# Performance work log

Measured on AMD Instinct MI355X. Metric: run time of the kernel, lower is better.

## Reference

```python
import jax, jax.numpy as jnp
import numpy as np

BATCH = 4096
DIM = 512
TEMP = 0.5

def setup_inputs() -> dict:
    key = jax.random.key(0)
    k1, k2 = jax.random.split(key)
    emb_i = jax.random.normal(k1, (BATCH, DIM), dtype=jnp.float32)
    emb_j = jax.random.normal(k2, (BATCH, DIM), dtype=jnp.float32)
    return {"emb_i": emb_i, "emb_j": emb_j}

def reference(emb_i, emb_j):
    n = emb_i.shape[0]
    # L2-normalize once (torch F.normalize uses eps=1e-12 clamp on norm)
    z_i = emb_i / jnp.maximum(jnp.linalg.norm(emb_i, axis=1, keepdims=True), 1e-12)
    z_j = emb_j / jnp.maximum(jnp.linalg.norm(emb_j, axis=1, keepdims=True), 1e-12)
    z = jnp.concatenate([z_i, z_j], axis=0)            # [2N, D]
    sim = jnp.einsum('nd,md->nm', z, z)                # cosine sim, single GEMM
    # positives: diag(sim, +N) and diag(sim, -N) == rowwise dot(z_i, z_j)
    pos_ij = jnp.sum(z_i * z_j, axis=1)                # [N]
    positives = jnp.concatenate([pos_ij, pos_ij], 0)   # [2N]
    exp_sim = jnp.exp(sim / TEMP)
    mask = 1.0 - jnp.eye(2 * n, dtype=sim.dtype)
    denom = jnp.sum(mask * exp_sim, axis=1)            # [2N]
    loss_partial = -(positives / TEMP - jnp.log(denom))
    return jnp.sum(loss_partial) / (2 * n)
```

## Files before the change

### kernel.cpp

```cpp
#include <hip/hip_runtime.h>
#include <hip/hip_bf16.h>

#define N_ROWS 4096
#define DIM 512
#define TWO_N 8192
#define NTILE 64
#define NTRI  (NTILE * (NTILE + 1) / 2)

typedef __bf16 bf16x8 __attribute__((ext_vector_type(8)));
typedef float  f32x4  __attribute__((ext_vector_type(4)));

__device__ inline unsigned short f2bf(float f) {
    unsigned int u = __float_as_uint(f);
    u += 0x7fffu + ((u >> 16) & 1u);
    return (unsigned short)(u >> 16);
}

__device__ inline void g2l16(const void* g, void* l) {
    __builtin_amdgcn_global_load_lds(
        (const __attribute__((address_space(1))) void*)g,
        (__attribute__((address_space(3))) void*)l,
        16, 0, 0);
}

__global__ void normalize_kernel(const float* __restrict__ ei,
                                 const float* __restrict__ ej,
                                 unsigned short* __restrict__ zb,
                                 float* __restrict__ pos,
                                 float* __restrict__ denom,
                                 float* __restrict__ out) {
    int r = blockIdx.x;
    int t = threadIdx.x;
    const float2 vi = ((const float2*)(ei + (size_t)r * DIM))[t];
    const float2 vj = ((const float2*)(ej + (size_t)r * DIM))[t];
    float si  = vi.x * vi.x + vi.y * vi.y;
    float sj  = vj.x * vj.x + vj.y * vj.y;
    float sij = vi.x * vj.x + vi.y * vj.y;

    for (int o = 32; o; o >>= 1) {
        si  += __shfl_down(si, o);
        sj  += __shfl_down(sj, o);
        sij += __shfl_down(sij, o);
    }
    __shared__ float red[3][4];
    int wave = t >> 6, lane = t & 63;
    if (lane == 0) { red[0][wave] = si; red[1][wave] = sj; red[2][wave] = sij; }
    __syncthreads();
    si  = red[0][0] + red[0][1] + red[0][2] + red[0][3];
    sj  = red[1][0] + red[1][1] + red[1][2] + red[1][3];
    sij = red[2][0] + red[2][1] + red[2][2] + red[2][3];

    float rni = 1.0f / fmaxf(sqrtf(si), 1e-12f);
    float rnj = 1.0f / fmaxf(sqrtf(sj), 1e-12f);
    if (t == 0) {
        pos[r] = sij * rni * rnj;
        denom[r] = 0.0f;
        denom[r + N_ROWS] = 0.0f;
        if (r == 0) out[0] = 0.0f;
    }
    ushort2 zi2 = make_ushort2(f2bf(vi.x * rni), f2bf(vi.y * rni));
    ushort2 zj2 = make_ushort2(f2bf(vj.x * rnj), f2bf(vj.y * rnj));
    ((ushort2*)(zb + (size_t)r * DIM))[t] = zi2;
    ((ushort2*)(zb + (size_t)(r + N_ROWS) * DIM))[t] = zj2;
}

__global__ __launch_bounds__(256, 4) void gemm_exp_kernel(
        const unsigned short* __restrict__ zb,
        float* __restrict__ denom) {
    const int w = blockIdx.x;
    const int t = (w & 7) * (NTRI / 8) + (w >> 3);
    int by = (int)(0.5f * (2.0f * NTILE + 1.0f -
              sqrtf((2.0f * NTILE + 1.0f) * (2.0f * NTILE + 1.0f) - 8.0f * t)));
    while ((by + 1) * NTILE - ((by + 1) * by) / 2 <= t) ++by;
    while (by * NTILE - (by * (by - 1)) / 2 > t) --by;
    const int bx = by + (t - (by * NTILE - (by * (by - 1)) / 2));

    const int rb = by * 128, cb = bx * 128;
    const bool diag = (rb == cb);

    const int tid  = threadIdx.x;
    const int wave = tid >> 6;
    const int lane = tid & 63;
    const int quad = lane >> 4;
    const int m    = lane & 15;
    const int wm   = (wave >> 1) * 64;
    const int wn   = (wave & 1) * 64;

    __shared__ __align__(16) unsigned short As[128 * 64];
    __shared__ __align__(16) unsigned short Bs[128 * 64];

    f32x4 acc[4][4];
    #pragma unroll
    for (int i = 0; i < 4; ++i)
        #pragma unroll
        for (int j = 0; j < 4; ++j)
            #pragma unroll
            for (int r = 0; r < 4; ++r) acc[i][j][r] = 0.0f;

    const int srow8 = lane >> 3;
    const int sk    = (((lane & 7) ^ srow8) * 8);

    for (int it = 0; it < DIM / 64; ++it) {
        if (it) __syncthreads();
        const int k0 = it * 64;
        #pragma unroll
        for (int cc = 0; cc < 4; ++cc) {
            int c   = 4 * wave + cc;
            int row = c * 8 + srow8;
            g2l16(zb + (size_t)(rb + row) * DIM + k0 + sk, As + c * 512);
            g2l16(zb + (size_t)(cb + row) * DIM + k0 + sk, Bs + c * 512);
        }
        __syncthreads();

        #pragma unroll
        for (int h = 0; h < 2; ++h) {
            bf16x8 af[4], bfr[4];
            const int sl = ((((h << 2) | quad) ^ (m & 7)) * 8);
            #pragma unroll
            for (int i = 0; i < 4; ++i)
                af[i] = *(const bf16x8*)(As + (wm + i * 16 + m) * 64 + sl);
            #pragma unroll
            for (int j = 0; j < 4; ++j)
                bfr[j] = *(const bf16x8*)(Bs + (wn + j * 16 + m) * 64 + sl);

            #pragma unroll
            for (int i = 0; i < 4; ++i)
                #pragma unroll
                for (int j = 0; j < 4; ++j)
                    acc[i][j] = __builtin_amdgcn_mfma_f32_16x16x32_bf16(
                        af[i], bfr[j], acc[i][j], 0, 0, 0);
        }
    }

    __syncthreads();

    float* rs = (float*)As;
    float* cs = rs + 128;
    if (tid < 128) { rs[tid] = 0.0f; cs[tid] = 0.0f; }
    __syncthreads();

    float colsum[4] = {0.0f, 0.0f, 0.0f, 0.0f};
    #pragma unroll
    for (int i = 0; i < 4; ++i) {
        #pragma unroll
        for (int r = 0; r < 4; ++r) {
            int lrow = wm + i * 16 + quad * 4 + r;
            int grow = rb + lrow;
            float s = 0.0f;
            #pragma unroll
            for (int j = 0; j < 4; ++j) {
                int gcol = cb + wn + j * 16 + m;
                float v  = __expf(2.0f * acc[i][j][r]);
                v = (grow == gcol) ? 0.0f : v;
                s += v;
                colsum[j] += v;
            }
            s += __shfl_xor(s, 1);
            s += __shfl_xor(s, 2);
            s += __shfl_xor(s, 4);
            s += __shfl_xor(s, 8);
            if (m == 0) atomicAdd(&rs[lrow], s);
        }
    }
    if (!diag) {
        #pragma unroll
        for (int j = 0; j < 4; ++j) {
            float s = colsum[j];
            s += __shfl_xor(s, 16);
            s += __shfl_xor(s, 32);
            if (quad == 0) atomicAdd(&cs[wn + j * 16 + m], s);
        }
    }
    __syncthreads();
    if (tid < 128) {
        atomicAdd(&denom[rb + tid], rs[tid]);
        if (!diag) atomicAdd(&denom[cb + tid], cs[tid]);
    }
}

__global__ void loss_kernel(const float* __restrict__ pos,
                            const float* __restrict__ denom,
                            float* __restrict__ out) {
    int r = blockIdx.x * 256 + threadIdx.x;
    float s = __logf(denom[r]) - 2.0f * pos[r & (N_ROWS - 1)];
    for (int o = 32; o; o >>= 1) s += __shfl_down(s, o);
    __shared__ float red[4];
    int t = threadIdx.x;
    if ((t & 63) == 0) red[t >> 6] = s;
    __syncthreads();
    if (t == 0)
        atomicAdd(out, (red[0] + red[1] + red[2] + red[3]) / (float)TWO_N);
}

extern "C" void kernel_launch(void* const* d_in, const int* in_sizes, int n_in,
                              void* d_out, int out_size, void* d_ws, size_t ws_size,
                              hipStream_t stream) {
    const float* ei = (const float*)d_in[0];
    const float* ej = (const float*)d_in[1];

    unsigned short* zb  = (unsigned short*)d_ws;
    float* pos   = (float*)((char*)d_ws + (size_t)TWO_N * DIM * sizeof(unsigned short));
    float* denom = pos + N_ROWS;
    float* out   = (float*)d_out;

    normalize_kernel<<<N_ROWS, 256, 0, stream>>>(ei, ej, zb, pos, denom, out);
    gemm_exp_kernel<<<NTRI, 256, 0, stream>>>(zb, denom);
    loss_kernel<<<TWO_N / 256, 256, 0, stream>>>(pos, denom, out);
}
```

Measured before the change: 119.2 us.

## Quantize normalized embeddings to FP8 and use FP8 MFMA for similarity GEMM

Normalized embeddings are now stored as FP8 (e4m3 via cvt_pk_fp8) instead of BF16. The GEMM uses 16x16x32 fp8 MFMA with a 128-byte K tile, so there are half as many K iterations, and global and LDS traffic is halved. The trade is lower precision in the cosine similarities. Because the values are exponentiated with 1/T = 2, the loss may drift beyond tolerance.

```diff
diff --git a/kernel.cpp b/kernel.cpp
--- a/kernel.cpp
+++ b/kernel.cpp
@@ -7,14 +7,7 @@
 #define NTILE 64
 #define NTRI  (NTILE * (NTILE + 1) / 2)
 
-typedef __bf16 bf16x8 __attribute__((ext_vector_type(8)));
-typedef float  f32x4  __attribute__((ext_vector_type(4)));
-
-__device__ inline unsigned short f2bf(float f) {
-    unsigned int u = __float_as_uint(f);
-    u += 0x7fffu + ((u >> 16) & 1u);
-    return (unsigned short)(u >> 16);
-}
+typedef float f32x4 __attribute__((ext_vector_type(4)));
 
 __device__ inline void g2l16(const void* g, void* l) {
     __builtin_amdgcn_global_load_lds(
@@ -25,7 +18,7 @@
 
 __global__ void normalize_kernel(const float* __restrict__ ei,
                                  const float* __restrict__ ej,
-                                 unsigned short* __restrict__ zb,
+                                 unsigned char* __restrict__ zq,
                                  float* __restrict__ pos,
                                  float* __restrict__ denom,
                                  float* __restrict__ out) {
@@ -58,14 +51,14 @@
         denom[r + N_ROWS] = 0.0f;
         if (r == 0) out[0] = 0.0f;
     }
-    ushort2 zi2 = make_ushort2(f2bf(vi.x * rni), f2bf(vi.y * rni));
-    ushort2 zj2 = make_ushort2(f2bf(vj.x * rnj), f2bf(vj.y * rnj));
-    ((ushort2*)(zb + (size_t)r * DIM))[t] = zi2;
-    ((ushort2*)(zb + (size_t)(r + N_ROWS) * DIM))[t] = zj2;
+    int pi8 = __builtin_amdgcn_cvt_pk_fp8_f32(vi.x * rni, vi.y * rni, 0, false);
+    int pj8 = __builtin_amdgcn_cvt_pk_fp8_f32(vj.x * rnj, vj.y * rnj, 0, false);
+    ((unsigned short*)(zq + (size_t)r * DIM))[t] = (unsigned short)pi8;
+    ((unsigned short*)(zq + (size_t)(r + N_ROWS) * DIM))[t] = (unsigned short)pj8;
 }
 
 __global__ __launch_bounds__(256, 4) void gemm_exp_kernel(
-        const unsigned short* __restrict__ zb,
+        const unsigned char* __restrict__ zq,
         float* __restrict__ denom) {
     const int w = blockIdx.x;
     const int t = (w & 7) * (NTRI / 8) + (w >> 3);
@@ -86,8 +79,8 @@
     const int wm   = (wave >> 1) * 64;
     const int wn   = (wave & 1) * 64;
 
-    __shared__ __align__(16) unsigned short As[128 * 64];
-    __shared__ __align__(16) unsigned short Bs[128 * 64];
+    __shared__ __align__(16) unsigned char As[128 * 128];
+    __shared__ __align__(16) unsigned char Bs[128 * 128];
 
     f32x4 acc[4][4];
     #pragma unroll
@@ -98,36 +91,37 @@
             for (int r = 0; r < 4; ++r) acc[i][j][r] = 0.0f;
 
     const int srow8 = lane >> 3;
-    const int sk    = (((lane & 7) ^ srow8) * 8);
-
-    for (int it = 0; it < DIM / 64; ++it) {
+    const int sk    = (((lane & 7) ^ srow8) * 16);
+
+    for (int it = 0; it < 4; ++it) {
         if (it) __syncthreads();
-        const int k0 = it * 64;
+        const int k0 = it * 128;
         #pragma unroll
         for (int cc = 0; cc < 4; ++cc) {
             int c   = 4 * wave + cc;
             int row = c * 8 + srow8;
-            g2l16(zb + (size_t)(rb + row) * DIM + k0 + sk, As + c * 512);
-            g2l16(zb + (size_t)(cb + row) * DIM + k0 + sk, Bs + c * 512);
+            g2l16(zq + (size_t)(rb + row) * DIM + k0 + sk, As + c * 1024);
+            g2l16(zq + (size_t)(cb + row) * DIM + k0 + sk, Bs + c * 1024);
         }
         __syncthreads();
 
         #pragma unroll
-        for (int h = 0; h < 2; ++h) {
-            bf16x8 af[4], bfr[4];
-            const int sl = ((((h << 2) | quad) ^ (m & 7)) * 8);
+        for (int kk = 0; kk < 4; ++kk) {
+            const int s8 = kk * 4 + quad;
+            const int sl = (((s8 >> 1) ^ (m & 7)) * 16) + (s8 & 1) * 8;
+            long long af[4], bfr[4];
             #pragma unroll
             for (int i = 0; i < 4; ++i)
-                af[i] = *(const bf16x8*)(As + (wm + i * 16 + m) * 64 + sl);
+                af[i] = *(const long long*)(As + (wm + i * 16 + m) * 128 + sl);
             #pragma unroll
             for (int j = 0; j < 4; ++j)
-                bfr[j] = *(const bf16x8*)(Bs + (wn + j * 16 + m) * 64 + sl);
+                bfr[j] = *(const long long*)(Bs + (wn + j * 16 + m) * 128 + sl);
 
             #pragma unroll
             for (int i = 0; i < 4; ++i)
                 #pragma unroll
                 for (int j = 0; j < 4; ++j)
-                    acc[i][j] = __builtin_amdgcn_mfma_f32_16x16x32_bf16(
+                    acc[i][j] = __builtin_amdgcn_mfma_f32_16x16x32_fp8_fp8(
                         af[i], bfr[j], acc[i][j], 0, 0, 0);
         }
     }
@@ -198,12 +192,12 @@
     const float* ei = (const float*)d_in[0];
     const float* ej = (const float*)d_in[1];
 
-    unsigned short* zb  = (unsigned short*)d_ws;
-    float* pos   = (float*)((char*)d_ws + (size_t)TWO_N * DIM * sizeof(unsigned short));
+    unsigned char* zq = (unsigned char*)d_ws;
+    float* pos   = (float*)((char*)d_ws + (size_t)TWO_N * DIM);
     float* denom = pos + N_ROWS;
     float* out   = (float*)d_out;
 
-    normalize_kernel<<<N_ROWS, 256, 0, stream>>>(ei, ej, zb, pos, denom, out);
-    gemm_exp_kernel<<<NTRI, 256, 0, stream>>>(zb, denom);
+    normalize_kernel<<<N_ROWS, 256, 0, stream>>>(ei, ej, zq, pos, denom, out);
+    gemm_exp_kernel<<<NTRI, 256, 0, stream>>>(zq, denom);
     loss_kernel<<<TWO_N / 256, 256, 0, stream>>>(pos, denom, out);
 }
```

New measurement: 107.2 us. 10.0% less time.
